# Performance work log

Hardware: AMD Instinct MI355X
Metric: run time of the kernel (lower is better)

Reference implementation:

```python
import jax, jax.numpy as jnp
import numpy as np

K = 7        # kernal_size
STRIDE = 1
PAD = 3      # padding (reflect)
M = K // 2   # center tap index
GAMA = 0.5
EPS = 1e-09


def interp_linear(x, n_out):
    # torch F.interpolate(mode='linear', align_corners=False) on last dim. x: (b, c, n_in)
    n_in = x.shape[-1]
    src = (jnp.arange(n_out, dtype=jnp.float32) + 0.5) * (n_in / n_out) - 0.5
    src = jnp.clip(src, 0.0, n_in - 1.0)
    lo = jnp.floor(src).astype(jnp.int32)
    hi = jnp.minimum(lo + 1, n_in - 1)
    w = (src - lo.astype(jnp.float32)).astype(x.dtype)
    return x[..., lo] * (1.0 - w) + x[..., hi] * w


def unfold1d(x, k, s, p):
    # x: (b, c, n) -> windows (b, L, c, k), matching F.unfold's c-major/k-minor layout
    if p > 0:
        x = jnp.pad(x, ((0, 0), (0, 0), (p, p)), mode='reflect')
    n = x.shape[-1]
    L = (n - k) // s + 1
    idx = jnp.arange(L)[:, None] * s + jnp.arange(k)[None, :]  # (L, k)
    win = x[:, :, idx]                                          # (b, c, L, k)
    return jnp.transpose(win, (0, 2, 1, 3))                     # (b, L, c, k)


def setup_inputs() -> dict:
    key = jax.random.key(0)
    k1, k2, k3, k4, k5 = jax.random.split(key, 5)
    b, dc, nd = 16, 16, 1024
    c_in, c_out, n = 64, 128, 4096
    deep = jax.random.normal(k1, (b, dc, nd), dtype=jnp.float32)
    x = jax.random.normal(k2, (b, c_in, n), dtype=jnp.float32)
    conv_w = jax.random.normal(k3, (c_in, dc), dtype=jnp.float32) * (1.0 / np.sqrt(dc))
    conv_b = jax.random.normal(k4, (c_in,), dtype=jnp.float32) * 0.02
    fc_w = jax.random.normal(k5, (c_out, c_in * K), dtype=jnp.float32) * (1.0 / np.sqrt(c_in * K))
    return {"deep": deep, "x": x, "conv_w": conv_w, "conv_b": conv_b, "fc_w": fc_w}


def reference(deep, x, conv_w, conv_b, fc_w):
    b, c, n = x.shape
    # --- get_deep_loss ---
    xr = interp_linear(deep, n)                                  # (b, dc, n)
    y = jnp.einsum('bdn,cd->bcn', xr, conv_w) + conv_b[None, :, None]
    mean = jnp.mean(y, axis=2, keepdims=True)
    var = jnp.var(y, axis=2, keepdims=True, ddof=1)              # torch var_mean unbiased
    xs = GAMA * (y - mean) / (var + EPS)                         # DeepShuffle1d
    x1 = unfold1d(xs, K, STRIDE, PAD)                            # (b, L, c, k)
    d = jnp.abs(x1 - x1[..., M:M + 1])
    loss = 1.0 - jnp.tanh(d) ** 2                                # (b, L, c, k)
    alpha = 1.0 / jnp.sum(loss, axis=-1, keepdims=True)          # (b, L, c, 1)
    deep_loss = (loss * alpha).reshape(b, -1, c * K)             # (b, L, c*k)
    # --- deep_conv ---
    y1 = unfold1d(x, K, STRIDE, PAD).reshape(b, -1, c * K)       # (b, L, c*k)
    out = jnp.einsum('blf,of->bol', deep_loss * y1, fc_w)        # (b, c_out, L)
    return out
```

## Files before the change

### kernel.cpp

```cpp
#include <hip/hip_runtime.h>
#include <hip/hip_bf16.h>
#include <math.h>

namespace {
typedef __attribute__((ext_vector_type(8)))  short  short8;
typedef __attribute__((ext_vector_type(4)))  float  floatx4;

constexpr int Bc = 16;
constexpr int DC = 16;
constexpr int ND = 1024;
constexpr int C  = 64;
constexpr int N  = 4096;
constexpr int CO = 128;
constexpr int KW = 7;
constexpr int F  = C * KW;
constexpr int LT = 32;
constexpr int PLD = F + 8;
constexpr int GPS = 560;
constexpr int NS = F / 32;

constexpr size_t WB_OFF = 0;
constexpr size_t GP_OFF = 131072;
constexpr size_t MC_OFF = 417792;
constexpr size_t SC_OFF = 421888;

constexpr float EXP2_SCALE = 2.8853900817779268f;

__device__ inline unsigned short f2bf(float f) {
    __hip_bfloat16 h = __float2bfloat16(f);
    return __builtin_bit_cast(unsigned short, h);
}
__device__ inline float rcpf(float x) { return __builtin_amdgcn_rcpf(x); }

__global__ __launch_bounds__(256)
void k0(const float* __restrict__ deep, const float* __restrict__ fcw,
        unsigned short* __restrict__ wbs, float* __restrict__ gp)
{
    __shared__ __align__(16) float Dch[DC][132];
    const int blk = blockIdx.x;
    const int tid = threadIdx.x;

    if (blk < 28) {
        const int g    = blk * 256 + tid;
        const int lane = g & 63;
        const int q    = lane >> 4;
        const int rr   = lane & 15;
        const int rest = g >> 6;
        const int t    = rest & 1;
        const int sw   = rest >> 1;
        const int s    = sw % NS;
        const int w    = sw / NS;
        const int o    = w * 32 + t * 16 + rr;
        const int f    = s * 32 + q * 8;
        const float4 v0 = *(const float4*)(fcw + o * F + f);
        const float4 v1 = *(const float4*)(fcw + o * F + f + 4);
        short8 h;
        h[0] = (short)f2bf(v0.x); h[1] = (short)f2bf(v0.y);
        h[2] = (short)f2bf(v0.z); h[3] = (short)f2bf(v0.w);
        h[4] = (short)f2bf(v1.x); h[5] = (short)f2bf(v1.y);
        h[6] = (short)f2bf(v1.z); h[7] = (short)f2bf(v1.w);
        ((short8*)wbs)[g] = h;
        return;
    }
    const int i2 = blk - 28;
    const int b  = i2 >> 3;
    const int ch = i2 & 7;
    const int t0 = ch * 128;
    const int d  = tid >> 4;
    const int e  = tid & 15;
#pragma unroll
    for (int p = 0; p < 9; ++p) {
        const int tt = e + 16 * p;
        if (tt < 129)
            Dch[d][tt] = deep[(b * DC + d) * ND + min(t0 + tt, ND - 1)];
    }
    __syncthreads();
    float a0 = 0.f, a1 = 0.f, as = 0.f;
    const int n1 = (ch == 7) ? 127 : 128;
    for (int t = 0; t < 128; ++t) {
        const float vd  = Dch[d][t];
        const float ve  = Dch[e][t];
        const float ve1 = (t < n1) ? Dch[e][t + 1] : 0.f;
        a0 = fmaf(vd, ve, a0);
        a1 = fmaf(vd, ve1, a1);
        as += vd;
    }
    float* gpb = gp + (b * 8 + ch) * GPS;
    gpb[tid] = a0;
    gpb[256 + tid] = a1;
    if (e == 0) {
        gpb[512 + d] = as;
        if (ch == 0) gpb[528 + d] = Dch[d][0];
        if (ch == 7) gpb[544 + d] = Dch[d][127];
    }
}

__global__ __launch_bounds__(256)
void ks(const float* __restrict__ gp, const float* __restrict__ conv_w,
        const float* __restrict__ conv_b, float* __restrict__ mcs,
        float* __restrict__ scs)
{
    __shared__ float G0s[256], G1s[256], ss[16], dd0[16], ddN[16], qp[8][64];
    const int b = blockIdx.x, tid = threadIdx.x;
    {
        float a0 = 0.f, a1 = 0.f;
#pragma unroll
        for (int ch = 0; ch < 8; ++ch) {
            const float* gpb = gp + (b * 8 + ch) * GPS;
            a0 += gpb[tid];
            a1 += gpb[256 + tid];
        }
        G0s[tid] = a0; G1s[tid] = a1;
        if (tid < 16) {
            float s = 0.f;
#pragma unroll
            for (int ch = 0; ch < 8; ++ch) s += gp[(b * 8 + ch) * GPS + 512 + tid];
            ss[tid]  = s;
            dd0[tid] = gp[(b * 8 + 0) * GPS + 528 + tid];
            ddN[tid] = gp[(b * 8 + 7) * GPS + 544 + tid];
        }
    }
    __syncthreads();
    const int c = tid & 63, part = tid >> 6;
    float w[DC];
    {
        const float4* wr = (const float4*)(conv_w + c * DC);
#pragma unroll
        for (int p = 0; p < 4; ++p) {
            const float4 v = wr[p];
            w[4 * p] = v.x; w[4 * p + 1] = v.y; w[4 * p + 2] = v.z; w[4 * p + 3] = v.w;
        }
    }
    float q0 = 0.f, q1 = 0.f;
#pragma unroll
    for (int dd = 0; dd < 4; ++dd) {
        const int d = 4 * part + dd;
        float i0 = 0.f, i1 = 0.f;
#pragma unroll
        for (int e = 0; e < DC; ++e) {
            i0 = fmaf(w[e], G0s[d * 16 + e], i0);
            i1 = fmaf(w[e], G1s[d * 16 + e], i1);
        }
        q0 = fmaf(w[d], i0, q0);
        q1 = fmaf(w[d], i1, q1);
    }
    qp[part][c] = q0;
    qp[4 + part][c] = q1;
    __syncthreads();
    if (tid < 64) {
        const float Q0 = qp[0][c] + qp[1][c] + qp[2][c] + qp[3][c];
        const float Q1 = qp[4][c] + qp[5][c] + qp[6][c] + qp[7][c];
        float wS = 0.f, V0 = 0.f, VN = 0.f;
#pragma unroll
        for (int d = 0; d < DC; ++d) {
            wS = fmaf(w[d], ss[d],  wS);
            V0 = fmaf(w[d], dd0[d], V0);
            VN = fmaf(w[d], ddN[d], VN);
        }
        const float cb   = conv_b[c];
        const float mean = wS * (1.f / 1024.f) + cb;
        const float S2   = 2.625f * Q0 + 1.375f * Q1 + 0.6875f * (V0 * V0 + VN * VN)
                         + 8.f * cb * wS + 4096.f * cb * cb;
        const float var  = (S2 - 4096.f * mean * mean) * (1.f / 4095.f);
        mcs[b * 64 + c] = wS * (1.f / 1024.f);
        scs[b * 64 + c] = (0.5f / (var + 1e-9f)) * EXP2_SCALE;
    }
}

__global__ __launch_bounds__(256, 3)
void k2(const float* __restrict__ deep, const float* __restrict__ conv_w,
        const float* __restrict__ x, const float* __restrict__ mcs,
        const float* __restrict__ scs, const unsigned short* __restrict__ wbs,
        float* __restrict__ out)
{
    __shared__ __align__(16) unsigned short phi[LT * PLD];
    __shared__ __align__(16) float Dw[12 * 16];
    const int b   = blockIdx.y;
    const int l0  = blockIdx.x * LT;
    const int t0  = l0 >> 2;
    const int tid = threadIdx.x;
    const int c   = tid & 63;
    const int seg = tid >> 6;

    if (tid < 192) {
        const int ti = tid >> 4, d = tid & 15;
        const int t = min(max(t0 - 2 + ti, 0), ND - 1);
        Dw[ti * 16 + d] = deep[(b * DC + d) * ND + t];
    }
    float w[DC];
    {
        const float4* wr = (const float4*)(conv_w + c * DC);
#pragma unroll
        for (int p = 0; p < 4; ++p) {
            const float4 v = wr[p];
            w[4 * p] = v.x; w[4 * p + 1] = v.y; w[4 * p + 2] = v.z; w[4 * p + 3] = v.w;
        }
    }
    const float mc  = mcs[b * 64 + c];
    const float sc2 = scs[b * 64 + c];
    __syncthreads();

    {
        const int base = l0 + seg * 8;
        float Vr[6];
#pragma unroll
        for (int m = 0; m < 6; ++m) {
            const float* dr = Dw + (2 * seg + m) * 16;
            float a = 0.f;
#pragma unroll
            for (int d = 0; d < DC; ++d) a = fmaf(w[d], dr[d], a);
            Vr[m] = a;
        }
        const float WA[4] = {0.375f, 0.125f, 0.875f, 0.625f};
        float xsv[14], xvf[14];
        const bool edge = (blockIdx.x == 0 && seg == 0) ||
                          (blockIdx.x == (N / LT - 1) && seg == 3);
        const float* xr = x + (size_t)(b * C + c) * N;
        if (!edge) {
            const float4 x0 = *(const float4*)(xr + base - 4);
            const float4 x1 = *(const float4*)(xr + base);
            const float4 x2 = *(const float4*)(xr + base + 4);
            const float4 x3 = *(const float4*)(xr + base + 8);
            const float xf[16] = {x0.x, x0.y, x0.z, x0.w, x1.x, x1.y, x1.z, x1.w,
                                  x2.x, x2.y, x2.z, x2.w, x3.x, x3.y, x3.z, x3.w};
#pragma unroll
            for (int i = 0; i < 14; ++i) {
                const int r  = (i + 1) & 3;
                const int ma = ((i + 5) >> 2) - 1 + (r >> 1);
                const float wa = WA[r];
                xsv[i] = (fmaf(wa, Vr[ma], (1.f - wa) * Vr[ma + 1]) - mc) * sc2;
                xvf[i] = xf[1 + i];
            }
        } else {
            const int tbase = t0 + 2 * seg - 2;
#pragma unroll
            for (int i = 0; i < 14; ++i) {
                const int j  = base - 3 + i;
                const int ja = (j < 0) ? -j : j;
                const int jr = min(ja, 2 * N - 2 - ja);
                const int t  = jr >> 2;
                const int r  = jr & 3;
                const float wa = WA[r];
                int tA = t - 1 + (r >> 1);
                int tB = tA + 1;
                if (tA < 0) { tA = 0; tB = 0; }
                if (tB > ND - 1) tB = ND - 1;
                const int ia = tA - tbase;
                const int ib = tB - tbase;
                xsv[i] = (wa * Vr[ia] + (1.f - wa) * Vr[ib] - mc) * sc2;
                xvf[i] = xr[jr];
            }
        }
        unsigned short* pcol = phi + c * KW;
#pragma unroll
        for (int li = 0; li < 8; ++li) {
            const float cen = xsv[li + 3];
            float u[KW];
            float s = 0.25f;
            u[3] = 0.25f;
#pragma unroll
            for (int k = 0; k < KW; ++k) {
                if (k == 3) continue;
                const float d = fabsf(xsv[li + k] - cen);
                const float e = __builtin_amdgcn_exp2f(-d);
                const float t = 1.f + e;
                const float uk = e * rcpf(t * t);
                u[k] = uk;
                s += uk;
            }
            const float al = rcpf(s);
            unsigned short* pr = pcol + (seg * 8 + li) * PLD;
#pragma unroll
            for (int k = 0; k < KW; ++k) pr[k] = f2bf(u[k] * al * xvf[li + k]);
        }
    }
    __syncthreads();

    const int lane = tid & 63;
    const int quad = lane >> 4;
    const int rr   = lane & 15;
    const int o0   = seg * 32;

    floatx4 acc00 = {0.f, 0.f, 0.f, 0.f}, acc01 = acc00, acc10 = acc00, acc11 = acc00;
    const short8* wp = (const short8*)wbs + (size_t)seg * (NS * 2 * 64) + lane;
    const unsigned short* prow0 = phi + rr * PLD + quad * 8;
    const unsigned short* prow1 = prow0 + 16 * PLD;

#pragma unroll
    for (int s = 0; s < NS; ++s) {
        const int f0 = 32 * s;
        const short8 a0 = wp[s * 128];
        const short8 a1 = wp[s * 128 + 64];
        const short8 b0 = *(const short8*)(prow0 + f0);
        const short8 b1 = *(const short8*)(prow1 + f0);
        acc00 = __builtin_amdgcn_mfma_f32_16x16x32_bf16(a0, b0, acc00, 0, 0, 0);
        acc01 = __builtin_amdgcn_mfma_f32_16x16x32_bf16(a0, b1, acc01, 0, 0, 0);
        acc10 = __builtin_amdgcn_mfma_f32_16x16x32_bf16(a1, b0, acc10, 0, 0, 0);
        acc11 = __builtin_amdgcn_mfma_f32_16x16x32_bf16(a1, b1, acc11, 0, 0, 0);
    }

    float* ob = out + (size_t)(b * CO) * N + l0;
#pragma unroll
    for (int i = 0; i < 4; ++i) {
        const int om = quad * 4 + i;
        ob[(o0 + om) * N      + rr     ] = acc00[i];
        ob[(o0 + om) * N      + 16 + rr] = acc01[i];
        ob[(o0 + 16 + om) * N + rr     ] = acc10[i];
        ob[(o0 + 16 + om) * N + 16 + rr] = acc11[i];
    }
}
}

extern "C" void kernel_launch(void* const* d_in, const int* in_sizes, int n_in,
                              void* d_out, int out_size, void* d_ws, size_t ws_size,
                              hipStream_t stream)
{
    const float* deep   = (const float*)d_in[0];
    const float* x      = (const float*)d_in[1];
    const float* conv_w = (const float*)d_in[2];
    const float* conv_b = (const float*)d_in[3];
    const float* fc_w   = (const float*)d_in[4];
    float* out = (float*)d_out;

    unsigned short* wbuf = (unsigned short*)((char*)d_ws + WB_OFF);
    float*          gp   = (float*)((char*)d_ws + GP_OFF);
    float*          mcs  = (float*)((char*)d_ws + MC_OFF);
    float*          scs  = (float*)((char*)d_ws + SC_OFF);

    hipLaunchKernelGGL(k0, dim3(28 + 128), dim3(256), 0, stream,
                       deep, fc_w, wbuf, gp);
    hipLaunchKernelGGL(ks, dim3(Bc), dim3(256), 0, stream,
                       gp, conv_w, conv_b, mcs, scs);
    hipLaunchKernelGGL(k2, dim3(N / LT, Bc), dim3(256), 0, stream,
                       deep, conv_w, x, mcs, scs, wbuf, out);
}
```

Measured before the change: 119.1 us.

## Pad feature dimension from 7 to 8 taps per channel for vectorized phi stores

Changes the reduction layout so each input channel occupies 8 bf16 slots (7 taps plus a zero) in both the packed weight buffer and the shared-memory phi tile. Each output row can then be written to LDS as one 16-byte short8 store instead of seven scalar 2-byte stores. In exchange the MFMA reduction grows from 14 to 16 k-steps, doing more matrix work on zeros. The x global loads are also hoisted above the barrier so they overlap the deep-window staging.

Result: faster. 115.7 us (-2.9%).

```diff
diff --git a/kernel.cpp b/kernel.cpp
--- a/kernel.cpp
+++ b/kernel.cpp
@@ -14,15 +14,16 @@
 constexpr int CO = 128;
 constexpr int KW = 7;
 constexpr int F  = C * KW;
+constexpr int F2 = C * 8;
 constexpr int LT = 32;
-constexpr int PLD = F + 8;
+constexpr int PLD = F2 + 8;
 constexpr int GPS = 560;
-constexpr int NS = F / 32;
+constexpr int NS = F2 / 32;
 
 constexpr size_t WB_OFF = 0;
-constexpr size_t GP_OFF = 131072;
-constexpr size_t MC_OFF = 417792;
-constexpr size_t SC_OFF = 421888;
+constexpr size_t GP_OFF = 262144;
+constexpr size_t MC_OFF = 548864;
+constexpr size_t SC_OFF = 552960;
 
 constexpr float EXP2_SCALE = 2.8853900817779268f;
 
@@ -40,7 +41,7 @@
     const int blk = blockIdx.x;
     const int tid = threadIdx.x;
 
-    if (blk < 28) {
+    if (blk < 32) {
         const int g    = blk * 256 + tid;
         const int lane = g & 63;
         const int q    = lane >> 4;
@@ -48,21 +49,22 @@
         const int rest = g >> 6;
         const int t    = rest & 1;
         const int sw   = rest >> 1;
-        const int s    = sw % NS;
-        const int w    = sw / NS;
+        const int s    = sw & 15;
+        const int w    = sw >> 4;
         const int o    = w * 32 + t * 16 + rr;
-        const int f    = s * 32 + q * 8;
-        const float4 v0 = *(const float4*)(fcw + o * F + f);
-        const float4 v1 = *(const float4*)(fcw + o * F + f + 4);
+        const int c    = s * 4 + q;
+        const float* src = fcw + o * F + c * KW;
+        const float4 v0 = *(const float4*)(src);
+        const float4 v1 = *(const float4*)(src + 3);
         short8 h;
         h[0] = (short)f2bf(v0.x); h[1] = (short)f2bf(v0.y);
         h[2] = (short)f2bf(v0.z); h[3] = (short)f2bf(v0.w);
-        h[4] = (short)f2bf(v1.x); h[5] = (short)f2bf(v1.y);
-        h[6] = (short)f2bf(v1.z); h[7] = (short)f2bf(v1.w);
+        h[4] = (short)f2bf(v1.y); h[5] = (short)f2bf(v1.z);
+        h[6] = (short)f2bf(v1.w); h[7] = 0;
         ((short8*)wbs)[g] = h;
         return;
     }
-    const int i2 = blk - 28;
+    const int i2 = blk - 32;
     const int b  = i2 >> 3;
     const int ch = i2 & 7;
     const int t0 = ch * 128;
@@ -198,10 +200,25 @@
     }
     const float mc  = mcs[b * 64 + c];
     const float sc2 = scs[b * 64 + c];
+
+    const int base = l0 + seg * 8;
+    const bool edge = (blockIdx.x == 0 && seg == 0) ||
+                      (blockIdx.x == (N / LT - 1) && seg == 3);
+    const float* xr = x + (size_t)(b * C + c) * N;
+    float xf[16];
+    if (!edge) {
+        const float4 x0 = *(const float4*)(xr + base - 4);
+        const float4 x1 = *(const float4*)(xr + base);
+        const float4 x2 = *(const float4*)(xr + base + 4);
+        const float4 x3 = *(const float4*)(xr + base + 8);
+        xf[0]=x0.x; xf[1]=x0.y; xf[2]=x0.z; xf[3]=x0.w;
+        xf[4]=x1.x; xf[5]=x1.y; xf[6]=x1.z; xf[7]=x1.w;
+        xf[8]=x2.x; xf[9]=x2.y; xf[10]=x2.z; xf[11]=x2.w;
+        xf[12]=x3.x; xf[13]=x3.y; xf[14]=x3.z; xf[15]=x3.w;
+    }
     __syncthreads();
 
     {
-        const int base = l0 + seg * 8;
         float Vr[6];
 #pragma unroll
         for (int m = 0; m < 6; ++m) {
@@ -213,16 +230,7 @@
         }
         const float WA[4] = {0.375f, 0.125f, 0.875f, 0.625f};
         float xsv[14], xvf[14];
-        const bool edge = (blockIdx.x == 0 && seg == 0) ||
-                          (blockIdx.x == (N / LT - 1) && seg == 3);
-        const float* xr = x + (size_t)(b * C + c) * N;
         if (!edge) {
-            const float4 x0 = *(const float4*)(xr + base - 4);
-            const float4 x1 = *(const float4*)(xr + base);
-            const float4 x2 = *(const float4*)(xr + base + 4);
-            const float4 x3 = *(const float4*)(xr + base + 8);
-            const float xf[16] = {x0.x, x0.y, x0.z, x0.w, x1.x, x1.y, x1.z, x1.w,
-                                  x2.x, x2.y, x2.z, x2.w, x3.x, x3.y, x3.z, x3.w};
 #pragma unroll
             for (int i = 0; i < 14; ++i) {
                 const int r  = (i + 1) & 3;
@@ -251,7 +259,7 @@
                 xvf[i] = xr[jr];
             }
         }
-        unsigned short* pcol = phi + c * KW;
+        unsigned short* pcol = phi + c * 8;
 #pragma unroll
         for (int li = 0; li < 8; ++li) {
             const float cen = xsv[li + 3];
@@ -269,9 +277,11 @@
                 s += uk;
             }
             const float al = rcpf(s);
-            unsigned short* pr = pcol + (seg * 8 + li) * PLD;
-#pragma unroll
-            for (int k = 0; k < KW; ++k) pr[k] = f2bf(u[k] * al * xvf[li + k]);
+            short8 ph;
+#pragma unroll
+            for (int k = 0; k < KW; ++k) ph[k] = (short)f2bf(u[k] * al * xvf[li + k]);
+            ph[7] = 0;
+            *(short8*)(pcol + (seg * 8 + li) * PLD) = ph;
         }
     }
     __syncthreads();
@@ -327,7 +337,7 @@
     float*          mcs  = (float*)((char*)d_ws + MC_OFF);
     float*          scs  = (float*)((char*)d_ws + SC_OFF);
 
-    hipLaunchKernelGGL(k0, dim3(28 + 128), dim3(256), 0, stream,
+    hipLaunchKernelGGL(k0, dim3(32 + 128), dim3(256), 0, stream,
                        deep, fc_w, wbuf, gp);
     hipLaunchKernelGGL(ks, dim3(Bc), dim3(256), 0, stream,
                        gp, conv_w, conv_b, mcs, scs);
```
